# Kernel optimization log

Measured on AMD Instinct MI355X. Metric: run time of the kernel, lower is better.

Reference implementation:

```python
import jax, jax.numpy as jnp
import numpy as np

N_NODES = 100000
N_EDGES = 3200000
N_GRAPHS = 512
IN_DIM = 29   # NUM_COMPONENT_TYPES(15) + NUM_PARAMS(14)
HID = 128
LAT = 256


def setup_inputs() -> dict:
    key = jax.random.key(0)
    ks = jax.random.split(key, 16)
    x = jax.random.normal(ks[0], (N_NODES, IN_DIM), dtype=jnp.float32)
    edge_index = jax.random.randint(ks[1], (2, N_EDGES), 0, N_NODES, dtype=jnp.int64)
    batch = jnp.sort(jax.random.randint(ks[2], (N_NODES,), 0, N_GRAPHS, dtype=jnp.int64))

    def lin(k, fan_in, fan_out):
        kw, kb = jax.random.split(k)
        s = 1.0 / np.sqrt(fan_in)
        W = jax.random.uniform(kw, (fan_in, fan_out), minval=-s, maxval=s, dtype=jnp.float32)
        b = jax.random.uniform(kb, (fan_out,), minval=-s, maxval=s, dtype=jnp.float32)
        return W, b

    W1, b1 = lin(ks[3], IN_DIM, HID)
    W2, b2 = lin(ks[4], HID, HID)
    W3, b3 = lin(ks[5], HID, HID)
    Wmu, bmu = lin(ks[6], HID, LAT)
    Wlv, blv = lin(ks[7], HID, LAT)
    return {"x": x, "edge_index": edge_index, "batch": batch,
            "W1": W1, "b1": b1, "W2": W2, "b2": b2, "W3": W3, "b3": b3,
            "Wmu": Wmu, "bmu": bmu, "Wlv": Wlv, "blv": blv}


def _gcn_conv(h, W, b, src, dst, dis):
    # PyG GCNConv: out = D^-1/2 (A + I) D^-1/2 (h W) + b
    hw = h @ W                                   # [N, out]
    norm = dis[src] * dis[dst]                   # [E]
    agg = jax.ops.segment_sum(hw[src] * norm[:, None], dst, num_segments=h.shape[0])
    return agg + hw * (dis * dis)[:, None] + b   # self-loop term has norm dis[i]^2


def reference(x, edge_index, batch, W1, b1, W2, b2, W3, b3, Wmu, bmu, Wlv, blv):
    src, dst = edge_index[0], edge_index[1]
    # symmetric degree with self-loops (computed once, identical across layers)
    deg = jax.ops.segment_sum(jnp.ones(src.shape[0], jnp.float32), dst,
                              num_segments=x.shape[0]) + 1.0
    dis = jax.lax.rsqrt(deg)

    h = jax.nn.relu(_gcn_conv(x, W1, b1, src, dst, dis))
    h = jax.nn.relu(_gcn_conv(h, W2, b2, src, dst, dis))
    h = jax.nn.relu(_gcn_conv(h, W3, b3, src, dst, dis))

    # global_mean_pool over graph ids
    sums = jax.ops.segment_sum(h, batch, num_segments=N_GRAPHS)
    cnts = jax.ops.segment_sum(jnp.ones(h.shape[0], jnp.float32), batch,
                               num_segments=N_GRAPHS)
    pooled = sums / jnp.maximum(cnts, 1.0)[:, None]   # [G, HID]

    mu = pooled @ Wmu + bmu
    logvar = pooled @ Wlv + blv
    return (mu, logvar)
```

## Files before the change

### kernel.cpp

```cpp
#include <hip/hip_runtime.h>
#include <hip/hip_bf16.h>

#define N_NODES 100000
#define N_EDGES 3200000
#define N_GRAPHS 512
#define IN_DIM 29
#define HID 128
#define LAT 256
#define NB 391
#define CAP 9216

typedef unsigned int uint;
typedef unsigned short ushort;
typedef float v4f __attribute__((ext_vector_type(4)));
typedef short v8s __attribute__((ext_vector_type(8)));

__device__ __forceinline__ ushort f2bf(float f) {
    uint u = __float_as_uint(f);
    return (ushort)((u + 0x7FFFu + ((u >> 16) & 1u)) >> 16);
}
__device__ __forceinline__ float bf2f(ushort h) { return __uint_as_float(((uint)h) << 16); }
__device__ __forceinline__ float bf_lo(uint p) { return __uint_as_float(p << 16); }
__device__ __forceinline__ float bf_hi(uint p) { return __uint_as_float(p & 0xFFFF0000u); }
__device__ __forceinline__ uint pack2(float a, float b) {
    return (uint)f2bf(a) | ((uint)f2bf(b) << 16);
}

__device__ __forceinline__ void bfadd(float* a, uint4 q) {
    a[0] += bf_lo(q.x); a[1] += bf_hi(q.x);
    a[2] += bf_lo(q.y); a[3] += bf_hi(q.y);
    a[4] += bf_lo(q.z); a[5] += bf_hi(q.z);
    a[6] += bf_lo(q.w); a[7] += bf_hi(q.w);
}

__device__ __forceinline__ v4f bf4(uint2 q) {
    return (v4f){bf_lo(q.x), bf_hi(q.x), bf_lo(q.y), bf_hi(q.y)};
}


__global__ __launch_bounds__(1024, 2) void k_binA(const int* __restrict__ src, const int* __restrict__ dst,
                                                  int* __restrict__ bktCnt, int* __restrict__ packed, int e) {
    __shared__ int hist[NB];
    __shared__ int base[NB];
    int t = threadIdx.x;
    for (int i = t; i < NB; i += 1024) hist[i] = 0;
    __syncthreads();
    int d[8], s[8];
    const int blockStart = blockIdx.x * 8192;
    #pragma unroll
    for (int k = 0; k < 8; ++k) {
        int idx = blockStart + k * 1024 + t;
        if (idx < e) {
            d[k] = dst[idx];
            s[k] = src[idx];
            atomicAdd(&hist[d[k] >> 8], 1);
        } else d[k] = -1;
    }
    __syncthreads();
    for (int i = t; i < NB; i += 1024) {
        int c = hist[i];
        base[i] = c ? atomicAdd(&bktCnt[i], c) : 0;
    }
    __syncthreads();
    #pragma unroll
    for (int k = 0; k < 8; ++k) {
        if (d[k] >= 0) {
            int b = d[k] >> 8;
            int pos = atomicAdd(&base[b], 1);
            if (pos < CAP) packed[b * CAP + pos] = ((d[k] & 255) << 17) | s[k];
        }
    }
}

__global__ __launch_bounds__(1024, 2) void k_binB(const int* __restrict__ bktCnt,
                                                  const int* __restrict__ packed, int* __restrict__ col,
                                                  int* __restrict__ rp, float* __restrict__ dis,
                                                  const float* __restrict__ x, ushort* __restrict__ xt16, int n) {
    __shared__ int cnt[8192];
    __shared__ int sh[1024];
    __shared__ float sdis[256];
    const int b = blockIdx.x;
    int cntB = bktCnt[b];
    if (cntB > CAP) cntB = CAP;
    const int segS = b * CAP;
    int t = threadIdx.x;
    int part = 0;
    for (int i = t; i < b; i += 1024) {
        int c = bktCnt[i];
        part += (c > CAP) ? CAP : c;
    }
    #pragma unroll
    for (int k = 0; k < 8; ++k) cnt[t + k * 1024] = 0;
    sh[t] = part;
    __syncthreads();
    for (int off = 512; off > 0; off >>= 1) {
        if (t < off) sh[t] += sh[t + off];
        __syncthreads();
    }
    const int colBase = sh[0];
    for (int j = t; j < cntB; j += 1024) {
        int pk = packed[segS + j];
        int key = ((pk >> 17) << 5) | ((pk & 0x1FFFF) >> 12);
        atomicAdd(&cnt[key], 1);
    }
    __syncthreads();
    int base8 = t << 3;
    int v[8];
    int sum = 0;
    #pragma unroll
    for (int k = 0; k < 8; ++k) { v[k] = cnt[base8 + k]; sum += v[k]; }
    sh[t] = sum;
    __syncthreads();
    for (int off = 1; off < 1024; off <<= 1) {
        int x2 = (t >= off) ? sh[t - off] : 0;
        __syncthreads();
        sh[t] += x2;
        __syncthreads();
    }
    int run = colBase + sh[t] - sum;
    #pragma unroll
    for (int k = 0; k < 8; ++k) { cnt[base8 + k] = run; run += v[k]; }
    __syncthreads();
    if (t < 256) {
        int node = (b << 8) + t;
        int start = cnt[t << 5];
        int next = (t == 255) ? (colBase + cntB) : cnt[(t + 1) << 5];
        int deg = next - start;
        float dv = rsqrtf((float)deg + 1.0f);
        sdis[t] = dv;
        if (node <= n) rp[node] = start;
        if (node < n) dis[node] = dv;
    }
    __syncthreads();
    for (int idx = t; idx < 256 * 32; idx += 1024) {
        int loc = idx >> 5;
        int node = (b << 8) + loc;
        if (node < n) {
            int k = idx & 31;
            float vv = (k < IN_DIM) ? x[(size_t)node * IN_DIM + k] * sdis[loc] : 0.f;
            xt16[((size_t)node << 5) + k] = f2bf(vv);
        }
    }
    for (int j = t; j < cntB; j += 1024) {
        int pk = packed[segS + j];
        int key = ((pk >> 17) << 5) | ((pk & 0x1FFFF) >> 12);
        int pos = atomicAdd(&cnt[key], 1);
        col[pos] = pk & 0x1FFFF;
    }
}


__device__ __forceinline__ void pack_one(const float* W, ushort* hi, ushort* lo, int Ksrc, int idx) {
    int j = idx & 7;
    int lane = (idx >> 3) & 63;
    int nt = (idx >> 9) & 7;
    int ks = idx >> 12;
    int k = ks * 32 + (lane >> 4) * 8 + j;
    int n = nt * 16 + (lane & 15);
    float v = (k < Ksrc) ? W[k * 128 + n] : 0.f;
    ushort h = f2bf(v);
    ushort l = f2bf(v - bf2f(h));
    hi[idx] = h;
    lo[idx] = l;
}

__global__ __launch_bounds__(256) void k_pack_all(const float* __restrict__ W1, const float* __restrict__ W2,
                                                  const float* __restrict__ W3,
                                                  ushort* w1h, ushort* w1l, ushort* w2h, ushort* w2l,
                                                  ushort* w3h, ushort* w3l, int* __restrict__ bktCnt) {
    int idx = blockIdx.x * 256 + threadIdx.x;
    if (idx < NB) bktCnt[idx] = 0;
    if (idx < 4096) {
        pack_one(W1, w1h, w1l, IN_DIM, idx);
    } else if (idx < 4096 + 16384) {
        pack_one(W2, w2h, w2l, HID, idx - 4096);
    } else if (idx < 4096 + 32768) {
        pack_one(W3, w3h, w3l, HID, idx - 4096 - 16384);
    }
}


__global__ __launch_bounds__(256, 6) void k_l1(const ushort* __restrict__ xt16, const int* __restrict__ rp,
                                               const int* __restrict__ col, const float* __restrict__ dis,
                                               const ushort* __restrict__ Whi, const ushort* __restrict__ Wlo,
                                               const float* __restrict__ bias, ushort* __restrict__ out, int n) {
    __shared__ float yl[32][36];
    int t = threadIdx.x;
    int loc = t >> 3;
    int node = blockIdx.x * 32 + loc;
    int c4 = (t & 7) << 2;
    if (node < n) {
        int s = rp[node], e = rp[node + 1];
        v4f A = (v4f){0.f, 0.f, 0.f, 0.f};
        v4f B = (v4f){0.f, 0.f, 0.f, 0.f};
        int j = s;
        for (; j + 7 < e; j += 8) {
            int c0 = col[j],     c1 = col[j + 1], c2 = col[j + 2], c3 = col[j + 3];
            int c4i = col[j + 4], c5 = col[j + 5], c6 = col[j + 6], c7 = col[j + 7];
            uint2 q0 = *(const uint2*)(xt16 + ((size_t)c0 << 5) + c4);
            uint2 q1 = *(const uint2*)(xt16 + ((size_t)c1 << 5) + c4);
            uint2 q2 = *(const uint2*)(xt16 + ((size_t)c2 << 5) + c4);
            uint2 q3 = *(const uint2*)(xt16 + ((size_t)c3 << 5) + c4);
            uint2 q4 = *(const uint2*)(xt16 + ((size_t)c4i << 5) + c4);
            uint2 q5 = *(const uint2*)(xt16 + ((size_t)c5 << 5) + c4);
            uint2 q6 = *(const uint2*)(xt16 + ((size_t)c6 << 5) + c4);
            uint2 q7 = *(const uint2*)(xt16 + ((size_t)c7 << 5) + c4);
            A += bf4(q0); B += bf4(q1); A += bf4(q2); B += bf4(q3);
            A += bf4(q4); B += bf4(q5); A += bf4(q6); B += bf4(q7);
        }
        if (j + 3 < e) {
            int c0 = col[j], c1 = col[j + 1], c2 = col[j + 2], c3 = col[j + 3];
            uint2 q0 = *(const uint2*)(xt16 + ((size_t)c0 << 5) + c4);
            uint2 q1 = *(const uint2*)(xt16 + ((size_t)c1 << 5) + c4);
            uint2 q2 = *(const uint2*)(xt16 + ((size_t)c2 << 5) + c4);
            uint2 q3 = *(const uint2*)(xt16 + ((size_t)c3 << 5) + c4);
            A += bf4(q0); B += bf4(q1); A += bf4(q2); B += bf4(q3);
            j += 4;
        }
        for (; j < e; ++j) {
            int c = col[j];
            A += bf4(*(const uint2*)(xt16 + ((size_t)c << 5) + c4));
        }
        A += bf4(*(const uint2*)(xt16 + ((size_t)node << 5) + c4));
        float dv = dis[node];
        v4f o = (A + B) * dv;
        yl[loc][c4 + 0] = o.x;
        yl[loc][c4 + 1] = o.y;
        yl[loc][c4 + 2] = o.z;
        yl[loc][c4 + 3] = o.w;
    }
    __syncthreads();
    const int wave = t >> 6;
    const int lane = t & 63;
    const int mrow = ((wave >> 1) << 4) + (lane & 15);
    const int ntBase = (wave & 1) * 4;
    const int kh = (lane >> 4) * 8;
    float a[8];
    #pragma unroll
    for (int j = 0; j < 8; ++j) a[j] = yl[mrow][kh + j];
    v8s ahi, alo;
    #pragma unroll
    for (int j = 0; j < 8; ++j) {
        ushort h = f2bf(a[j]);
        ushort l = f2bf(a[j] - bf2f(h));
        ahi[j] = (short)h;
        alo[j] = (short)l;
    }
    const ushort* bh = Whi + (size_t)lane * 8;
    const ushort* bl = Wlo + (size_t)lane * 8;
    v4f acc[4];
    #pragma unroll
    for (int i = 0; i < 4; ++i) acc[i] = (v4f){0.f, 0.f, 0.f, 0.f};
    #pragma unroll
    for (int i = 0; i < 4; ++i) {
        int nt = ntBase + i;
        v8s bhi = *(const v8s*)(bh + nt * 512);
        v8s blo = *(const v8s*)(bl + nt * 512);
        acc[i] = __builtin_amdgcn_mfma_f32_16x16x32_bf16(ahi, bhi, acc[i], 0, 0, 0);
        acc[i] = __builtin_amdgcn_mfma_f32_16x16x32_bf16(ahi, blo, acc[i], 0, 0, 0);
        acc[i] = __builtin_amdgcn_mfma_f32_16x16x32_bf16(alo, bhi, acc[i], 0, 0, 0);
    }
    const int col0 = lane & 15;
    const int orow0 = blockIdx.x * 32 + ((wave >> 1) << 4) + ((lane >> 4) << 2);
    float bb[4];
    #pragma unroll
    for (int i = 0; i < 4; ++i) bb[i] = bias[(ntBase + i) * 16 + col0];
    #pragma unroll
    for (int r = 0; r < 4; ++r) {
        int orow = orow0 + r;
        if (orow < n) {
            #pragma unroll
            for (int i = 0; i < 4; ++i)
                out[(size_t)orow * 128 + (ntBase + i) * 16 + col0] = f2bf(fmaxf(acc[i][r] + bb[i], 0.f));
        }
    }
}


__global__ __launch_bounds__(256, 4) void k_gemm_bf32(const ushort* __restrict__ in,
                                                      const ushort* __restrict__ Whi,
                                                      const ushort* __restrict__ Wlo,
                                                      const float* __restrict__ dis,
                                                      ushort* __restrict__ out, int n) {
    const int wave = threadIdx.x >> 6;
    const int lane = threadIdx.x & 63;
    const int m0 = (blockIdx.x * 4 + wave) * 32;
    if (m0 >= n) return;
    int row0 = m0 + (lane & 15);
    int row1 = row0 + 16;
    if (row0 >= n) row0 = n - 1;
    if (row1 >= n) row1 = n - 1;
    const int kh = (lane >> 4) * 8;
    const ushort* rp0 = in + (size_t)row0 * 128 + kh;
    const ushort* rp1 = in + (size_t)row1 * 128 + kh;

    v4f acc0[8], acc1[8];
    #pragma unroll
    for (int t = 0; t < 8; ++t) {
        acc0[t] = (v4f){0.f, 0.f, 0.f, 0.f};
        acc1[t] = (v4f){0.f, 0.f, 0.f, 0.f};
    }

    #pragma unroll
    for (int ks = 0; ks < 4; ++ks) {
        v8s a0 = *(const v8s*)(rp0 + ks * 32);
        v8s a1 = *(const v8s*)(rp1 + ks * 32);
        const ushort* bh = Whi + (size_t)(ks * 8) * 512 + (size_t)lane * 8;
        const ushort* bl = Wlo + (size_t)(ks * 8) * 512 + (size_t)lane * 8;
        #pragma unroll
        for (int nt = 0; nt < 8; ++nt) {
            v8s bhi = *(const v8s*)(bh + nt * 512);
            v8s blo = *(const v8s*)(bl + nt * 512);
            acc0[nt] = __builtin_amdgcn_mfma_f32_16x16x32_bf16(a0, bhi, acc0[nt], 0, 0, 0);
            acc0[nt] = __builtin_amdgcn_mfma_f32_16x16x32_bf16(a0, blo, acc0[nt], 0, 0, 0);
            acc1[nt] = __builtin_amdgcn_mfma_f32_16x16x32_bf16(a1, bhi, acc1[nt], 0, 0, 0);
            acc1[nt] = __builtin_amdgcn_mfma_f32_16x16x32_bf16(a1, blo, acc1[nt], 0, 0, 0);
        }
    }

    const int col0 = lane & 15;
    const int orow0 = m0 + (lane >> 4) * 4;
    #pragma unroll
    for (int r = 0; r < 4; ++r) {
        int orow = orow0 + r;
        if (orow < n) {
            float dv = dis[orow];
            #pragma unroll
            for (int nt = 0; nt < 8; ++nt)
                out[(size_t)orow * 128 + nt * 16 + col0] = f2bf(acc0[nt][r] * dv);
        }
        int orow2 = orow + 16;
        if (orow2 < n) {
            float dv = dis[orow2];
            #pragma unroll
            for (int nt = 0; nt < 8; ++nt)
                out[(size_t)orow2 * 128 + nt * 16 + col0] = f2bf(acc1[nt][r] * dv);
        }
    }
}


__global__ __launch_bounds__(256, 6) void k_agg(const ushort* __restrict__ hws, const int* __restrict__ rp,
                                                const int* __restrict__ col, const float* __restrict__ dis,
                                                const float* __restrict__ bias, ushort* __restrict__ out, int n) {
    int g = blockIdx.x * 32 + (threadIdx.x >> 3);
    int node = (g < n) ? g : g - n;
    if (g >= 2 * n) return;
    int c8 = ((g < n) ? 0 : 64) + ((threadIdx.x & 7) << 3);
    int s = rp[node], e = rp[node + 1];
    float A[8] = {0.f, 0.f, 0.f, 0.f, 0.f, 0.f, 0.f, 0.f};
    float B[8] = {0.f, 0.f, 0.f, 0.f, 0.f, 0.f, 0.f, 0.f};
    int j = s;
    for (; j + 7 < e; j += 8) {
        int c0 = col[j],     c1 = col[j + 1], c2 = col[j + 2], c3 = col[j + 3];
        int c4 = col[j + 4], c5 = col[j + 5], c6 = col[j + 6], c7 = col[j + 7];
        uint4 q0 = *(const uint4*)(hws + ((size_t)c0 << 7) + c8);
        uint4 q1 = *(const uint4*)(hws + ((size_t)c1 << 7) + c8);
        uint4 q2 = *(const uint4*)(hws + ((size_t)c2 << 7) + c8);
        uint4 q3 = *(const uint4*)(hws + ((size_t)c3 << 7) + c8);
        uint4 q4 = *(const uint4*)(hws + ((size_t)c4 << 7) + c8);
        uint4 q5 = *(const uint4*)(hws + ((size_t)c5 << 7) + c8);
        uint4 q6 = *(const uint4*)(hws + ((size_t)c6 << 7) + c8);
        uint4 q7 = *(const uint4*)(hws + ((size_t)c7 << 7) + c8);
        bfadd(A, q0); bfadd(B, q1); bfadd(A, q2); bfadd(B, q3);
        bfadd(A, q4); bfadd(B, q5); bfadd(A, q6); bfadd(B, q7);
    }
    if (j + 3 < e) {
        int c0 = col[j], c1 = col[j + 1], c2 = col[j + 2], c3 = col[j + 3];
        uint4 q0 = *(const uint4*)(hws + ((size_t)c0 << 7) + c8);
        uint4 q1 = *(const uint4*)(hws + ((size_t)c1 << 7) + c8);
        uint4 q2 = *(const uint4*)(hws + ((size_t)c2 << 7) + c8);
        uint4 q3 = *(const uint4*)(hws + ((size_t)c3 << 7) + c8);
        bfadd(A, q0); bfadd(B, q1); bfadd(A, q2); bfadd(B, q3);
        j += 4;
    }
    for (; j < e; ++j) {
        int c = col[j];
        uint4 q = *(const uint4*)(hws + ((size_t)c << 7) + c8);
        bfadd(A, q);
    }
    uint4 qs = *(const uint4*)(hws + ((size_t)node << 7) + c8);
    bfadd(A, qs);
    float dv = dis[node];
    float4 bv0 = *(const float4*)(bias + c8);
    float4 bv1 = *(const float4*)(bias + c8 + 4);
    float r0 = fmaxf(dv * (A[0] + B[0]) + bv0.x, 0.f);
    float r1 = fmaxf(dv * (A[1] + B[1]) + bv0.y, 0.f);
    float r2 = fmaxf(dv * (A[2] + B[2]) + bv0.z, 0.f);
    float r3 = fmaxf(dv * (A[3] + B[3]) + bv0.w, 0.f);
    float r4 = fmaxf(dv * (A[4] + B[4]) + bv1.x, 0.f);
    float r5 = fmaxf(dv * (A[5] + B[5]) + bv1.y, 0.f);
    float r6 = fmaxf(dv * (A[6] + B[6]) + bv1.z, 0.f);
    float r7 = fmaxf(dv * (A[7] + B[7]) + bv1.w, 0.f);
    uint4 o;
    o.x = pack2(r0, r1);
    o.y = pack2(r2, r3);
    o.z = pack2(r4, r5);
    o.w = pack2(r6, r7);
    *(uint4*)(out + (size_t)node * 128 + c8) = o;
}


__global__ __launch_bounds__(256) void k_pool_head(const ushort* __restrict__ h, const int* __restrict__ batch,
                                                   const float* __restrict__ Wmu, const float* __restrict__ bmu,
                                                   const float* __restrict__ Wlv, const float* __restrict__ blv,
                                                   float* __restrict__ out, int n) {
    int g = blockIdx.x;
    int t = threadIdx.x;
    int lo = 0, hi = n;
    while (lo < hi) { int m = (lo + hi) >> 1; if (batch[m] < g) lo = m + 1; else hi = m; }
    int start = lo;
    hi = n;
    while (lo < hi) { int m = (lo + hi) >> 1; if (batch[m] < g + 1) lo = m + 1; else hi = m; }
    int end = lo;

    __shared__ float sh0[256];
    __shared__ float sh1[256];
    __shared__ float pooled[128];
    int lane = t & 63;
    int grp = t >> 6;
    float a0 = 0.f, a1 = 0.f;
    for (int i = start + grp; i < end; i += 4) {
        uint q = *(const uint*)(h + (size_t)i * 128 + lane * 2);
        a0 += bf_lo(q);
        a1 += bf_hi(q);
    }
    sh0[t] = a0;
    sh1[t] = a1;
    __syncthreads();
    if (t < 64) {
        float cnt = (float)(end - start);
        float inv = 1.0f / fmaxf(cnt, 1.0f);
        float s0 = sh0[t] + sh0[t + 64] + sh0[t + 128] + sh0[t + 192];
        float s1 = sh1[t] + sh1[t + 64] + sh1[t + 128] + sh1[t + 192];
        pooled[t * 2] = s0 * inv;
        pooled[t * 2 + 1] = s1 * inv;
    }
    __syncthreads();
    float amu = bmu[t], alv = blv[t];
    for (int k = 0; k < 128; k += 4) {
        float p0 = pooled[k], p1 = pooled[k + 1], p2 = pooled[k + 2], p3 = pooled[k + 3];
        amu += p0 * Wmu[(k + 0) * 256 + t] + p1 * Wmu[(k + 1) * 256 + t]
             + p2 * Wmu[(k + 2) * 256 + t] + p3 * Wmu[(k + 3) * 256 + t];
        alv += p0 * Wlv[(k + 0) * 256 + t] + p1 * Wlv[(k + 1) * 256 + t]
             + p2 * Wlv[(k + 2) * 256 + t] + p3 * Wlv[(k + 3) * 256 + t];
    }
    out[(size_t)g * 256 + t] = amu;
    out[(size_t)N_GRAPHS * 256 + (size_t)g * 256 + t] = alv;
}


extern "C" void kernel_launch(void* const* d_in, const int* in_sizes, int n_in,
                              void* d_out, int out_size, void* d_ws, size_t ws_size,
                              hipStream_t stream) {
    const float* x    = (const float*)d_in[0];
    const int*   eidx = (const int*)d_in[1];
    const int*   batch= (const int*)d_in[2];
    const float* W1   = (const float*)d_in[3];
    const float* b1   = (const float*)d_in[4];
    const float* W2   = (const float*)d_in[5];
    const float* b2   = (const float*)d_in[6];
    const float* W3   = (const float*)d_in[7];
    const float* b3   = (const float*)d_in[8];
    const float* Wmu  = (const float*)d_in[9];
    const float* bmu  = (const float*)d_in[10];
    const float* Wlv  = (const float*)d_in[11];
    const float* blv  = (const float*)d_in[12];
    float* out = (float*)d_out;

    const int N = N_NODES, E = N_EDGES;
    const int* srcp = eidx;
    const int* dstp = eidx + E;

    ushort* w1h = (ushort*)d_ws;
    ushort* w1l = w1h + 4096;
    ushort* w2h = w1l + 4096;
    ushort* w2l = w2h + 16384;
    ushort* w3h = w2l + 16384;
    ushort* w3l = w3h + 16384;
    ushort* A   = w3l + 16384;
    ushort* B   = A + (size_t)N * 128;
    float*  dis = (float*)(B + (size_t)N * 128);
    int*   rp   = (int*)(dis + N);
    int*   bktCnt   = rp + (N + 2);
    int*   colStart = bktCnt + 512;
    int*   packed = colStart + 512;
    int*   col    = packed + (size_t)NB * CAP;

    ushort* xt16 = A;

    const int gE8192 = (E + 8191) / 8192;

    k_pack_all<<<144, 256, 0, stream>>>(W1, W2, W3, w1h, w1l, w2h, w2l, w3h, w3l, bktCnt);

    k_binA<<<gE8192, 1024, 0, stream>>>(srcp, dstp, bktCnt, packed, E);
    k_binB<<<NB, 1024, 0, stream>>>(bktCnt, packed, col, rp, dis, x, xt16, N);

    const int gGemm2 = (N + 127) / 128;
    const int gL1    = (N + 31) / 32;
    const int gAgg   = (2 * N + 31) / 32;

    k_l1<<<gL1, 256, 0, stream>>>(xt16, rp, col, dis, w1h, w1l, b1, B, N);

    k_gemm_bf32<<<gGemm2, 256, 0, stream>>>(B, w2h, w2l, dis, A, N);
    k_agg<<<gAgg, 256, 0, stream>>>(A, rp, col, dis, b2, B, N);
    k_gemm_bf32<<<gGemm2, 256, 0, stream>>>(B, w3h, w3l, dis, A, N);
    k_agg<<<gAgg, 256, 0, stream>>>(A, rp, col, dis, b3, B, N);
    k_pool_head<<<N_GRAPHS, 256, 0, stream>>>(B, batch, Wmu, bmu, Wlv, blv, out, N);
}
```

Measured before the change: 449.0 us.

## Fuse final GCN aggregation with global mean pooling via atomics

New measurement: 432.3 us (median of 2 runs). 1.04x faster.

```diff
diff --git a/kernel.cpp b/kernel.cpp
--- a/kernel.cpp
+++ b/kernel.cpp
@@ -167,9 +167,11 @@
 __global__ __launch_bounds__(256) void k_pack_all(const float* __restrict__ W1, const float* __restrict__ W2,
                                                   const float* __restrict__ W3,
                                                   ushort* w1h, ushort* w1l, ushort* w2h, ushort* w2l,
-                                                  ushort* w3h, ushort* w3l, int* __restrict__ bktCnt) {
+                                                  ushort* w3h, ushort* w3l, int* __restrict__ bktCnt,
+                                                  float* __restrict__ pooled) {
     int idx = blockIdx.x * 256 + threadIdx.x;
     if (idx < NB) bktCnt[idx] = 0;
+    if (idx < N_GRAPHS * HID) pooled[idx] = 0.f;
     if (idx < 4096) {
         pack_one(W1, w1h, w1l, IN_DIM, idx);
     } else if (idx < 4096 + 16384) {
@@ -401,7 +403,81 @@
 }
 
 
-__global__ __launch_bounds__(256) void k_pool_head(const ushort* __restrict__ h, const int* __restrict__ batch,
+__global__ __launch_bounds__(256, 6) void k_agg_pool(const ushort* __restrict__ hws, const int* __restrict__ rp,
+                                                     const int* __restrict__ col, const float* __restrict__ dis,
+                                                     const float* __restrict__ bias, const int* __restrict__ batch,
+                                                     float* __restrict__ pooled, int n) {
+    __shared__ float red[256][8];
+    __shared__ int gID[32];
+    int t = threadIdx.x;
+    int g = blockIdx.x * 32 + (t >> 3);
+    int node = (g < n) ? g : g - n;
+    int half = (g < n) ? 0 : 1;
+    int c8 = half * 64 + ((t & 7) << 3);
+    int s = rp[node], e = rp[node + 1];
+    float A[8] = {0.f, 0.f, 0.f, 0.f, 0.f, 0.f, 0.f, 0.f};
+    float B[8] = {0.f, 0.f, 0.f, 0.f, 0.f, 0.f, 0.f, 0.f};
+    int j = s;
+    for (; j + 7 < e; j += 8) {
+        int c0 = col[j],     c1 = col[j + 1], c2 = col[j + 2], c3 = col[j + 3];
+        int c4 = col[j + 4], c5 = col[j + 5], c6 = col[j + 6], c7 = col[j + 7];
+        uint4 q0 = *(const uint4*)(hws + ((size_t)c0 << 7) + c8);
+        uint4 q1 = *(const uint4*)(hws + ((size_t)c1 << 7) + c8);
+        uint4 q2 = *(const uint4*)(hws + ((size_t)c2 << 7) + c8);
+        uint4 q3 = *(const uint4*)(hws + ((size_t)c3 << 7) + c8);
+        uint4 q4 = *(const uint4*)(hws + ((size_t)c4 << 7) + c8);
+        uint4 q5 = *(const uint4*)(hws + ((size_t)c5 << 7) + c8);
+        uint4 q6 = *(const uint4*)(hws + ((size_t)c6 << 7) + c8);
+        uint4 q7 = *(const uint4*)(hws + ((size_t)c7 << 7) + c8);
+        bfadd(A, q0); bfadd(B, q1); bfadd(A, q2); bfadd(B, q3);
+        bfadd(A, q4); bfadd(B, q5); bfadd(A, q6); bfadd(B, q7);
+    }
+    if (j + 3 < e) {
+        int c0 = col[j], c1 = col[j + 1], c2 = col[j + 2], c3 = col[j + 3];
+        uint4 q0 = *(const uint4*)(hws + ((size_t)c0 << 7) + c8);
+        uint4 q1 = *(const uint4*)(hws + ((size_t)c1 << 7) + c8);
+        uint4 q2 = *(const uint4*)(hws + ((size_t)c2 << 7) + c8);
+        uint4 q3 = *(const uint4*)(hws + ((size_t)c3 << 7) + c8);
+        bfadd(A, q0); bfadd(B, q1); bfadd(A, q2); bfadd(B, q3);
+        j += 4;
+    }
+    for (; j < e; ++j) {
+        int c = col[j];
+        uint4 q = *(const uint4*)(hws + ((size_t)c << 7) + c8);
+        bfadd(A, q);
+    }
+    uint4 qs = *(const uint4*)(hws + ((size_t)node << 7) + c8);
+    bfadd(A, qs);
+    float dv = dis[node];
+    float4 bv0 = *(const float4*)(bias + c8);
+    float4 bv1 = *(const float4*)(bias + c8 + 4);
+    red[t][0] = fmaxf(dv * (A[0] + B[0]) + bv0.x, 0.f);
+    red[t][1] = fmaxf(dv * (A[1] + B[1]) + bv0.y, 0.f);
+    red[t][2] = fmaxf(dv * (A[2] + B[2]) + bv0.z, 0.f);
+    red[t][3] = fmaxf(dv * (A[3] + B[3]) + bv0.w, 0.f);
+    red[t][4] = fmaxf(dv * (A[4] + B[4]) + bv1.x, 0.f);
+    red[t][5] = fmaxf(dv * (A[5] + B[5]) + bv1.y, 0.f);
+    red[t][6] = fmaxf(dv * (A[6] + B[6]) + bv1.z, 0.f);
+    red[t][7] = fmaxf(dv * (A[7] + B[7]) + bv1.w, 0.f);
+    if ((t & 7) == 0) gID[t >> 3] = batch[node];
+    __syncthreads();
+    if (t < 64) {
+        int lane8 = t >> 3, k = t & 7;
+        int g0 = gID[0], g1 = gID[31];
+        float s0 = 0.f, s1 = 0.f;
+        #pragma unroll 4
+        for (int gr = 0; gr < 32; ++gr) {
+            float v = red[(gr << 3) + lane8][k];
+            if (gID[gr] == g0) s0 += v; else s1 += v;
+        }
+        int ch = half * 64 + (lane8 << 3) + k;
+        atomicAdd(&pooled[(size_t)g0 * 128 + ch], s0);
+        if (g1 != g0) atomicAdd(&pooled[(size_t)g1 * 128 + ch], s1);
+    }
+}
+
+
+__global__ __launch_bounds__(256) void k_pool_head(const float* __restrict__ pooled, const int* __restrict__ batch,
                                                    const float* __restrict__ Wmu, const float* __restrict__ bmu,
                                                    const float* __restrict__ Wlv, const float* __restrict__ blv,
                                                    float* __restrict__ out, int n) {
@@ -414,32 +490,13 @@
     while (lo < hi) { int m = (lo + hi) >> 1; if (batch[m] < g + 1) lo = m + 1; else hi = m; }
     int end = lo;
 
-    __shared__ float sh0[256];
-    __shared__ float sh1[256];
-    __shared__ float pooled[128];
-    int lane = t & 63;
-    int grp = t >> 6;
-    float a0 = 0.f, a1 = 0.f;
-    for (int i = start + grp; i < end; i += 4) {
-        uint q = *(const uint*)(h + (size_t)i * 128 + lane * 2);
-        a0 += bf_lo(q);
-        a1 += bf_hi(q);
-    }
-    sh0[t] = a0;
-    sh1[t] = a1;
-    __syncthreads();
-    if (t < 64) {
-        float cnt = (float)(end - start);
-        float inv = 1.0f / fmaxf(cnt, 1.0f);
-        float s0 = sh0[t] + sh0[t + 64] + sh0[t + 128] + sh0[t + 192];
-        float s1 = sh1[t] + sh1[t + 64] + sh1[t + 128] + sh1[t + 192];
-        pooled[t * 2] = s0 * inv;
-        pooled[t * 2 + 1] = s1 * inv;
-    }
+    __shared__ float pl[128];
+    float inv = 1.0f / fmaxf((float)(end - start), 1.0f);
+    if (t < 128) pl[t] = pooled[(size_t)g * 128 + t] * inv;
     __syncthreads();
     float amu = bmu[t], alv = blv[t];
     for (int k = 0; k < 128; k += 4) {
-        float p0 = pooled[k], p1 = pooled[k + 1], p2 = pooled[k + 2], p3 = pooled[k + 3];
+        float p0 = pl[k], p1 = pl[k + 1], p2 = pl[k + 2], p3 = pl[k + 3];
         amu += p0 * Wmu[(k + 0) * 256 + t] + p1 * Wmu[(k + 1) * 256 + t]
              + p2 * Wmu[(k + 2) * 256 + t] + p3 * Wmu[(k + 3) * 256 + t];
         alv += p0 * Wlv[(k + 0) * 256 + t] + p1 * Wlv[(k + 1) * 256 + t]
@@ -486,12 +543,13 @@
     int*   colStart = bktCnt + 512;
     int*   packed = colStart + 512;
     int*   col    = packed + (size_t)NB * CAP;
+    float* pooled = (float*)(col + (size_t)E);
 
     ushort* xt16 = A;
 
     const int gE8192 = (E + 8191) / 8192;
 
-    k_pack_all<<<144, 256, 0, stream>>>(W1, W2, W3, w1h, w1l, w2h, w2l, w3h, w3l, bktCnt);
+    k_pack_all<<<256, 256, 0, stream>>>(W1, W2, W3, w1h, w1l, w2h, w2l, w3h, w3l, bktCnt, pooled);
 
     k_binA<<<gE8192, 1024, 0, stream>>>(srcp, dstp, bktCnt, packed, E);
     k_binB<<<NB, 1024, 0, stream>>>(bktCnt, packed, col, rp, dis, x, xt16, N);
@@ -505,6 +563,6 @@
     k_gemm_bf32<<<gGemm2, 256, 0, stream>>>(B, w2h, w2l, dis, A, N);
     k_agg<<<gAgg, 256, 0, stream>>>(A, rp, col, dis, b2, B, N);
     k_gemm_bf32<<<gGemm2, 256, 0, stream>>>(B, w3h, w3l, dis, A, N);
-    k_agg<<<gAgg, 256, 0, stream>>>(A, rp, col, dis, b3, B, N);
-    k_pool_head<<<N_GRAPHS, 256, 0, stream>>>(B, batch, Wmu, bmu, Wlv, blv, out, N);
-}
+    k_agg_pool<<<gAgg, 256, 0, stream>>>(A, rp, col, dis, b3, batch, pooled, N);
+    k_pool_head<<<N_GRAPHS, 256, 0, stream>>>(pooled, batch, Wmu, bmu, Wlv, blv, out, N);
+}
```
